# Optimization experiments

Measured on AMD Instinct MI355X. Metric: run time of the kernel, lower is better.

The kernel has to match this reference:

```python
import jax, jax.numpy as jnp
import numpy as np

D = 192   # token_dim == channel_dim == expert_dim == adapt_dim (required by source code)
S = 4096  # sequence length
NE = 8    # num_experts


def _ln(x, g, b, eps=1e-5):
    m = x.mean(-1, keepdims=True)
    v = ((x - m) ** 2).mean(-1, keepdims=True)
    return (x - m) / jnp.sqrt(v + eps) * g + b


def _adaptive(x, a, W, b, AW, Ab):
    # AdaptiveLinear with adapt_method='add': weight = W + adapt(a).view(out, in)
    dW = (AW @ a + Ab).reshape(W.shape)
    return x @ (W + dW).T + b


def setup_inputs() -> dict:
    key = jax.random.key(0)
    ks = iter(jax.random.split(key, 40))

    def n(shape, s=0.05):
        return jax.random.normal(next(ks), shape, dtype=jnp.float32) * s

    return {
        "x": n((1, S, D), 1.0),
        "W_in": n((D, D)), "b_in": n((D,)),
        "feat_W": n((D, D)), "feat_b": n((D,)),
        "feat_AW": n((D * D, D)), "feat_Ab": n((D * D,)),
        "an_g": jnp.ones((D,)), "an_b": jnp.zeros((D,)),
        "tm_W": n((D, D)), "tm_b": n((D,)),
        "tm_AW": n((D * D, D)), "tm_Ab": n((D * D,)),
        "tn_g": jnp.ones((D,)), "tn_b": jnp.zeros((D,)),
        "cm_W": n((D, D)), "cm_b": n((D,)),
        "cm_AW": n((D * D, D)), "cm_Ab": n((D * D,)),
        "cn_g": jnp.ones((D,)), "cn_b": jnp.zeros((D,)),
        "pm_W": n((D, D)), "pm_b": n((D,)),
        "gate_W": n((NE, D)), "gate_b": n((NE,)),
        "ex_W": n((NE, D, D)), "ex_b": n((NE, D)),
        "ex_AW": n((NE, D * D, D)), "ex_Ab": n((NE, D * D)),
        "mn_g": jnp.ones((D,)), "mn_b": jnp.zeros((D,)),
        "out_W": n((D, D)), "out_b": n((D,)),
    }


def reference(x, W_in, b_in, feat_W, feat_b, feat_AW, feat_Ab, an_g, an_b,
              tm_W, tm_b, tm_AW, tm_Ab, tn_g, tn_b,
              cm_W, cm_b, cm_AW, cm_Ab, cn_g, cn_b,
              pm_W, pm_b, gate_W, gate_b, ex_W, ex_b, ex_AW, ex_Ab,
              mn_g, mn_b, out_W, out_b):
    h = x @ W_in.T + b_in                                        # [1,S,D]
    xm = h.mean(axis=1)                                          # [1,D]
    a = _adaptive(xm, xm[0], feat_W, feat_b, feat_AW, feat_Ab)   # [1,D]
    a = _ln(a, an_g, an_b)
    a0 = a[0]                                                    # [D]
    t = _adaptive(h, a0, tm_W, tm_b, tm_AW, tm_Ab)               # token mixing
    t = _ln(t, tn_g, tn_b)
    c = _adaptive(t, a0, cm_W, cm_b, cm_AW, cm_Ab)               # channel mixing
    c = _ln(c, cn_g, cn_b)
    m = c @ pm_W.T + pm_b                                        # pre-MoE [1,S,D]
    gate = jax.nn.softmax(a @ gate_W.T + gate_b, axis=-1)[0]     # [NE]
    # batched hypernet weight generation for all experts at once
    dW = (jnp.einsum('eka,a->ek', ex_AW, a0) + ex_Ab).reshape(NE, D, D)
    We = ex_W + dW                                               # [NE,D,D]
    ye = jnp.einsum('bsd,ned->nbse', m, We) + ex_b[:, None, None, :]
    eo = jnp.einsum('n,nbse->bse', gate, ye)                     # soft-MoE sum
    eo = _ln(eo, mn_g, mn_b)
    eo = jax.nn.relu(eo)
    return eo @ out_W.T + out_b
```

## Files before the change

### kernel.cpp

```cpp
#include <hip/hip_runtime.h>

#define DD 192

template <int EMIT, int LNL>
__global__ __launch_bounds__(256) void stage2_k(
    const float* __restrict__ A, const float* __restrict__ W,
    const float* __restrict__ bias,
    const float* __restrict__ stats_in, const float* __restrict__ lng,
    const float* __restrict__ lnb,
    float* __restrict__ out, float* __restrict__ emit_buf) {
    __shared__ float WT[DD * 64];
    __shared__ float At[DD * 18];
    __shared__ float ms[16], rs[16];
    __shared__ float csum[4 * 64];

    const int t = threadIdx.x;
    const int tr = t >> 5, tc = t & 31;
    const int b = blockIdx.x;
    const int c0 = (b % 3) * 64;
    const int r0 = (b / 3) * 16;

    if (LNL > 0) {
        if (t < 16) {
            float s = stats_in[2 * (r0 + t)];
            float q = stats_in[2 * (r0 + t) + 1];
            float mean = s * (1.f / 192.f);
            float var = q * (1.f / 192.f) - mean * mean;
            ms[t] = mean;
            rs[t] = rsqrtf(var + 1e-5f);
        }
        __syncthreads();
    }

    {
        const float4* A4 = (const float4*)(A + (size_t)r0 * DD);
#pragma unroll
        for (int q = 0; q < 3; q++) {
            int fidx = t + 256 * q;
            int r = fidx / 48, jj = fidx - r * 48;
            float4 v = A4[fidx];
            if (LNL > 0) {
                float mean = ms[r], rstd = rs[r];
                float4 g4 = ((const float4*)lng)[jj];
                float4 b4 = ((const float4*)lnb)[jj];
                v.x = (v.x - mean) * rstd * g4.x + b4.x;
                v.y = (v.y - mean) * rstd * g4.y + b4.y;
                v.z = (v.z - mean) * rstd * g4.z + b4.z;
                v.w = (v.w - mean) * rstd * g4.w + b4.w;
                if (LNL == 2) {
                    v.x = fmaxf(v.x, 0.f); v.y = fmaxf(v.y, 0.f);
                    v.z = fmaxf(v.z, 0.f); v.w = fmaxf(v.w, 0.f);
                }
            }
            int j0 = 4 * jj;
            At[(j0 + 0) * 18 + r] = v.x;
            At[(j0 + 1) * 18 + r] = v.y;
            At[(j0 + 2) * 18 + r] = v.z;
            At[(j0 + 3) * 18 + r] = v.w;
        }
    }
    {
        const float4* W4 = (const float4*)(W + (size_t)c0 * DD);
#pragma unroll
        for (int q = 0; q < 12; q++) {
            int fidx = t + 256 * q;
            int ip = fidx / 48, jj = fidx - ip * 48;
            float4 v = W4[fidx];
            int j0 = 4 * jj;
            WT[(j0 + 0) * 64 + ((ip + 2 * ((j0 + 0) & 31)) & 63)] = v.x;
            WT[(j0 + 1) * 64 + ((ip + 2 * ((j0 + 1) & 31)) & 63)] = v.y;
            WT[(j0 + 2) * 64 + ((ip + 2 * ((j0 + 2) & 31)) & 63)] = v.z;
            WT[(j0 + 3) * 64 + ((ip + 2 * ((j0 + 3) & 31)) & 63)] = v.w;
        }
    }

    const int i0 = c0 + 2 * tc;
    float b0v = bias[i0], b1v = bias[i0 + 1];
    float acc00 = b0v, acc01 = b1v, acc10 = b0v, acc11 = b1v;
    __syncthreads();

#pragma unroll 4
    for (int j = 0; j < DD; j++) {
        float2 a2 = *(const float2*)&At[j * 18 + 2 * tr];
        int cs = (2 * tc + 2 * (j & 31)) & 63;
        float2 w2 = *(const float2*)&WT[j * 64 + cs];
        acc00 = fmaf(a2.x, w2.x, acc00);
        acc01 = fmaf(a2.x, w2.y, acc01);
        acc10 = fmaf(a2.y, w2.x, acc10);
        acc11 = fmaf(a2.y, w2.y, acc11);
    }

    const int ra = r0 + 2 * tr, rb = ra + 1;
    *(float2*)&out[(size_t)ra * DD + i0] = make_float2(acc00, acc01);
    *(float2*)&out[(size_t)rb * DD + i0] = make_float2(acc10, acc11);

    if (EMIT == 2) {
        float s0 = acc00 + acc01, q0 = acc00 * acc00 + acc01 * acc01;
        float s1 = acc10 + acc11, q1 = acc10 * acc10 + acc11 * acc11;
#pragma unroll
        for (int m = 16; m >= 1; m >>= 1) {
            s0 += __shfl_xor(s0, m); q0 += __shfl_xor(q0, m);
            s1 += __shfl_xor(s1, m); q1 += __shfl_xor(q1, m);
        }
        if (tc == 0) {
            atomicAdd(&emit_buf[2 * ra], s0);
            atomicAdd(&emit_buf[2 * ra + 1], q0);
            atomicAdd(&emit_buf[2 * rb], s1);
            atomicAdd(&emit_buf[2 * rb + 1], q1);
        }
    } else if (EMIT == 1) {
        float cs0 = acc00 + acc10;
        float cs1 = acc01 + acc11;
        cs0 += __shfl_xor(cs0, 32);
        cs1 += __shfl_xor(cs1, 32);
        int w = t >> 6;
        if ((t & 63) < 32) {
            csum[w * 64 + 2 * tc] = cs0;
            csum[w * 64 + 2 * tc + 1] = cs1;
        }
        __syncthreads();
        if (t < 64) {
            float s = csum[t] + csum[64 + t] + csum[128 + t] + csum[192 + t];
            atomicAdd(&emit_buf[c0 + t], s);
        }
    }
}

__global__ __launch_bounds__(256) void hyper_k(
    const float* __restrict__ tm_W, const float* __restrict__ tm_AW,
    const float* __restrict__ tm_Ab, const float* __restrict__ cm_W,
    const float* __restrict__ cm_AW, const float* __restrict__ cm_Ab,
    const float* __restrict__ ex_W, const float* __restrict__ ex_AW,
    const float* __restrict__ ex_Ab, const float* __restrict__ a0g,
    const float* __restrict__ gateg, float* __restrict__ Wt,
    float* __restrict__ Wc, float* __restrict__ Wmoe) {
    __shared__ float a0s[DD];
    __shared__ float rows[32 * 204];
    __shared__ float wb[32], ab[32], vals[32];
    const int t = threadIdx.x;
    const int b = blockIdx.x;
    const float* AW; const float* WB; const float* AB;
    int k0, mode, e = 0;
    if (b < 1152)      { mode = 0; AW = tm_AW; WB = tm_W; AB = tm_Ab; k0 = b * 32; }
    else if (b < 2304) { mode = 1; AW = cm_AW; WB = cm_W; AB = cm_Ab; k0 = (b - 1152) * 32; }
    else {
        mode = 2; int bb = b - 2304; e = bb / 1152; k0 = (bb - e * 1152) * 32;
        AW = ex_AW + (size_t)e * 36864 * DD;
        WB = ex_W + (size_t)e * 36864;
        AB = ex_Ab + (size_t)e * 36864;
    }
    if (t < DD) a0s[t] = a0g[t];
    if (t < 32) { wb[t] = WB[k0 + t]; ab[t] = AB[k0 + t]; }
    const float4* src4 = (const float4*)(AW + (size_t)k0 * DD);
#pragma unroll
    for (int q = 0; q < 6; q++) {
        int fidx = t + 256 * q;
        int r = fidx / 48, jj = fidx - r * 48;
        float4 v = src4[fidx];
        *(float4*)&rows[r * 204 + 4 * jj] = v;
    }
    __syncthreads();
    const int r = t >> 3, p = t & 7;
    float acc = 0.f;
#pragma unroll
    for (int q = 0; q < 6; q++) {
        int jo = p * 24 + 4 * q;
        float4 w = *(const float4*)&rows[r * 204 + jo];
        float4 aa = *(const float4*)&a0s[jo];
        acc = fmaf(w.x, aa.x, acc); acc = fmaf(w.y, aa.y, acc);
        acc = fmaf(w.z, aa.z, acc); acc = fmaf(w.w, aa.w, acc);
    }
    acc += __shfl_xor(acc, 1);
    acc += __shfl_xor(acc, 2);
    acc += __shfl_xor(acc, 4);
    if (p == 0) vals[r] = acc + wb[r] + ab[r];
    __syncthreads();
    if (t < 32) {
        if (mode == 0) Wt[k0 + t] = vals[t];
        else if (mode == 1) Wc[k0 + t] = vals[t];
        else atomicAdd(&Wmoe[k0 + t], gateg[e] * vals[t]);
    }
}

__global__ __launch_bounds__(256) void feat2_k(
    const float* __restrict__ feat_W, const float* __restrict__ feat_AW,
    const float* __restrict__ feat_Ab, const float* __restrict__ xm_sum,
    float* __restrict__ a_pre) {
    __shared__ float xms[DD];
    __shared__ float rows[32 * 204];
    __shared__ float wb[32], ab[32], vals[32];
    const int t = threadIdx.x;
    const int k0 = blockIdx.x * 32;
    if (t < DD) xms[t] = xm_sum[t] * (1.f / 4096.f);
    if (t < 32) { wb[t] = feat_W[k0 + t]; ab[t] = feat_Ab[k0 + t]; }
    const float4* src4 = (const float4*)(feat_AW + (size_t)k0 * DD);
#pragma unroll
    for (int q = 0; q < 6; q++) {
        int fidx = t + 256 * q;
        int r = fidx / 48, jj = fidx - r * 48;
        float4 v = src4[fidx];
        *(float4*)&rows[r * 204 + 4 * jj] = v;
    }
    __syncthreads();
    const int r = t >> 3, p = t & 7;
    float acc = 0.f;
#pragma unroll
    for (int q = 0; q < 6; q++) {
        int jo = p * 24 + 4 * q;
        float4 w = *(const float4*)&rows[r * 204 + jo];
        float4 aa = *(const float4*)&xms[jo];
        acc = fmaf(w.x, aa.x, acc); acc = fmaf(w.y, aa.y, acc);
        acc = fmaf(w.z, aa.z, acc); acc = fmaf(w.w, aa.w, acc);
    }
    acc += __shfl_xor(acc, 1);
    acc += __shfl_xor(acc, 2);
    acc += __shfl_xor(acc, 4);
    if (p == 0) vals[r] = acc + wb[r] + ab[r];
    __syncthreads();
    const int j0 = k0 % DD;
    if (t < 32) {
        float c = vals[t] * xms[j0 + t];
#pragma unroll
        for (int m = 16; m >= 1; m >>= 1) c += __shfl_xor(c, m);
        if (t == 0) atomicAdd(&a_pre[k0 / DD], c);
    }
}

__global__ __launch_bounds__(192) void vec_k(
    const float* __restrict__ a_pre, const float* __restrict__ feat_b,
    const float* __restrict__ an_g, const float* __restrict__ an_b,
    const float* __restrict__ gate_W, const float* __restrict__ gate_b,
    const float* __restrict__ ex_b, float* __restrict__ a0g,
    float* __restrict__ gateg, float* __restrict__ b_moe) {
    __shared__ float lgs[8];
    __shared__ float red[6];
    const int t = threadIdx.x;
    float v = a_pre[t] + feat_b[t];
    float s = v, q = v * v;
#pragma unroll
    for (int m = 32; m >= 1; m >>= 1) {
        s += __shfl_xor(s, m);
        q += __shfl_xor(q, m);
    }
    if ((t & 63) == 0) { red[t >> 6] = s; red[3 + (t >> 6)] = q; }
    if (t < 8) lgs[t] = gate_b[t];
    __syncthreads();
    float S = red[0] + red[1] + red[2];
    float Q = red[3] + red[4] + red[5];
    float mean = S * (1.f / 192.f);
    float var = Q * (1.f / 192.f) - mean * mean;
    float rstd = rsqrtf(var + 1e-5f);
    float a0v = (v - mean) * rstd * an_g[t] + an_b[t];
    a0g[t] = a0v;
#pragma unroll
    for (int e = 0; e < 8; e++) atomicAdd(&lgs[e], a0v * gate_W[e * DD + t]);
    __syncthreads();
    if (t == 0) {
        float mx = lgs[0];
        for (int e = 1; e < 8; e++) mx = fmaxf(mx, lgs[e]);
        float sum = 0.f, ex[8];
        for (int e = 0; e < 8; e++) { ex[e] = expf(lgs[e] - mx); sum += ex[e]; }
        for (int e = 0; e < 8; e++) lgs[e] = ex[e] / sum;
    }
    __syncthreads();
    if (t < 8) gateg[t] = lgs[t];
    float bm = 0.f;
#pragma unroll
    for (int e = 0; e < 8; e++) bm = fmaf(lgs[e], ex_b[e * DD + t], bm);
    b_moe[t] = bm;
}

extern "C" void kernel_launch(void* const* d_in, const int* in_sizes, int n_in,
                              void* d_out, int out_size, void* d_ws, size_t ws_size,
                              hipStream_t stream) {
    (void)in_sizes; (void)n_in; (void)out_size; (void)ws_size;
    const float* x       = (const float*)d_in[0];
    const float* W_in    = (const float*)d_in[1];
    const float* b_in    = (const float*)d_in[2];
    const float* feat_W  = (const float*)d_in[3];
    const float* feat_b  = (const float*)d_in[4];
    const float* feat_AW = (const float*)d_in[5];
    const float* feat_Ab = (const float*)d_in[6];
    const float* an_g    = (const float*)d_in[7];
    const float* an_b    = (const float*)d_in[8];
    const float* tm_W    = (const float*)d_in[9];
    const float* tm_b    = (const float*)d_in[10];
    const float* tm_AW   = (const float*)d_in[11];
    const float* tm_Ab   = (const float*)d_in[12];
    const float* tn_g    = (const float*)d_in[13];
    const float* tn_b    = (const float*)d_in[14];
    const float* cm_W    = (const float*)d_in[15];
    const float* cm_b    = (const float*)d_in[16];
    const float* cm_AW   = (const float*)d_in[17];
    const float* cm_Ab   = (const float*)d_in[18];
    const float* cn_g    = (const float*)d_in[19];
    const float* cn_b    = (const float*)d_in[20];
    const float* pm_W    = (const float*)d_in[21];
    const float* pm_b    = (const float*)d_in[22];
    const float* gate_W  = (const float*)d_in[23];
    const float* gate_b  = (const float*)d_in[24];
    const float* ex_W    = (const float*)d_in[25];
    const float* ex_b    = (const float*)d_in[26];
    const float* ex_AW   = (const float*)d_in[27];
    const float* ex_Ab   = (const float*)d_in[28];
    const float* mn_g    = (const float*)d_in[29];
    const float* mn_b    = (const float*)d_in[30];
    const float* out_W   = (const float*)d_in[31];
    const float* out_b   = (const float*)d_in[32];

    float* ws = (float*)d_ws;
    float* B0     = ws;
    float* B1     = ws + 786432;
    float* xm_sum = ws + 1572864;
    float* a_pre  = ws + 1573056;
    float* st1    = ws + 1573248;
    float* st2    = ws + 1581440;
    float* st3    = ws + 1589632;
    float* Wmoe   = ws + 1597824;
    float* Wt     = ws + 1634688;
    float* Wc     = ws + 1671552;
    float* a0     = ws + 1708416;
    float* gate   = ws + 1708608;
    float* b_moe  = ws + 1708616;

    hipMemsetAsync(xm_sum, 0, (size_t)61824 * sizeof(float), stream);

    stage2_k<1, 0><<<768, 256, 0, stream>>>(x, W_in, b_in, nullptr, nullptr, nullptr,
                                            B0, xm_sum);
    feat2_k<<<1152, 256, 0, stream>>>(feat_W, feat_AW, feat_Ab, xm_sum, a_pre);
    vec_k<<<1, 192, 0, stream>>>(a_pre, feat_b, an_g, an_b, gate_W, gate_b, ex_b,
                                 a0, gate, b_moe);
    hyper_k<<<11520, 256, 0, stream>>>(tm_W, tm_AW, tm_Ab, cm_W, cm_AW, cm_Ab,
                                       ex_W, ex_AW, ex_Ab, a0, gate, Wt, Wc, Wmoe);
    stage2_k<2, 0><<<768, 256, 0, stream>>>(B0, Wt, tm_b, nullptr, nullptr, nullptr,
                                            B1, st1);
    stage2_k<2, 1><<<768, 256, 0, stream>>>(B1, Wc, cm_b, st1, tn_g, tn_b, B0, st2);
    stage2_k<0, 1><<<768, 256, 0, stream>>>(B0, pm_W, pm_b, st2, cn_g, cn_b, B1, nullptr);
    stage2_k<2, 0><<<768, 256, 0, stream>>>(B1, Wmoe, b_moe, nullptr, nullptr, nullptr,
                                            B0, st3);
    stage2_k<0, 2><<<768, 256, 0, stream>>>(B0, out_W, out_b, st3, mn_g, mn_b,
                                            (float*)d_out, nullptr);
}
```

Measured before the change: 566.9 us.

## Double row tile to 32 and replace LN-stat atomics with per-column-group partials

The GEMM kernel now processes 32 rows per block, with each thread computing a 4x2 output tile, so each weight load from shared memory is reused across four rows and the grid halves to 384 blocks. The A tile is stored row-major with padding instead of transposed. Row sum and sum-of-squares statistics are written as three per-column-group partials and summed by the consumer, replacing the atomic adds. The memset shrinks accordingly. Costs are more shared memory per block, more registers, and fewer blocks, which lowers parallelism across the GPU's CUs.

```diff
diff --git a/kernel.cpp b/kernel.cpp
--- a/kernel.cpp
+++ b/kernel.cpp
@@ -3,27 +3,30 @@
 #define DD 192
 
 template <int EMIT, int LNL>
-__global__ __launch_bounds__(256) void stage2_k(
+__global__ __launch_bounds__(256) void stage3_k(
     const float* __restrict__ A, const float* __restrict__ W,
     const float* __restrict__ bias,
     const float* __restrict__ stats_in, const float* __restrict__ lng,
     const float* __restrict__ lnb,
     float* __restrict__ out, float* __restrict__ emit_buf) {
+    __shared__ float At[32 * 200];
     __shared__ float WT[DD * 64];
-    __shared__ float At[DD * 18];
-    __shared__ float ms[16], rs[16];
+    __shared__ float ms[32], rs[32];
     __shared__ float csum[4 * 64];
 
     const int t = threadIdx.x;
     const int tr = t >> 5, tc = t & 31;
     const int b = blockIdx.x;
-    const int c0 = (b % 3) * 64;
-    const int r0 = (b / 3) * 16;
+    const int cg = b % 3;
+    const int c0 = cg * 64;
+    const int r0 = (b / 3) * 32;
 
     if (LNL > 0) {
-        if (t < 16) {
-            float s = stats_in[2 * (r0 + t)];
-            float q = stats_in[2 * (r0 + t) + 1];
+        if (t < 32) {
+            int r = r0 + t;
+            float s = stats_in[2 * r] + stats_in[8192 + 2 * r] + stats_in[16384 + 2 * r];
+            float q = stats_in[2 * r + 1] + stats_in[8192 + 2 * r + 1]
+                    + stats_in[16384 + 2 * r + 1];
             float mean = s * (1.f / 192.f);
             float var = q * (1.f / 192.f) - mean * mean;
             ms[t] = mean;
@@ -35,10 +38,10 @@
     {
         const float4* A4 = (const float4*)(A + (size_t)r0 * DD);
 #pragma unroll
-        for (int q = 0; q < 3; q++) {
-            int fidx = t + 256 * q;
-            int r = fidx / 48, jj = fidx - r * 48;
-            float4 v = A4[fidx];
+        for (int q = 0; q < 6; q++) {
+            int f = t + 256 * q;
+            int r = f / 48, jj = f - r * 48;
+            float4 v = A4[f];
             if (LNL > 0) {
                 float mean = ms[r], rstd = rs[r];
                 float4 g4 = ((const float4*)lng)[jj];
@@ -52,20 +55,16 @@
                     v.z = fmaxf(v.z, 0.f); v.w = fmaxf(v.w, 0.f);
                 }
             }
-            int j0 = 4 * jj;
-            At[(j0 + 0) * 18 + r] = v.x;
-            At[(j0 + 1) * 18 + r] = v.y;
-            At[(j0 + 2) * 18 + r] = v.z;
-            At[(j0 + 3) * 18 + r] = v.w;
+            *(float4*)&At[r * 200 + 4 * jj] = v;
         }
     }
     {
         const float4* W4 = (const float4*)(W + (size_t)c0 * DD);
 #pragma unroll
         for (int q = 0; q < 12; q++) {
-            int fidx = t + 256 * q;
-            int ip = fidx / 48, jj = fidx - ip * 48;
-            float4 v = W4[fidx];
+            int f = t + 256 * q;
+            int ip = f / 48, jj = f - ip * 48;
+            float4 v = W4[f];
             int j0 = 4 * jj;
             WT[(j0 + 0) * 64 + ((ip + 2 * ((j0 + 0) & 31)) & 63)] = v.x;
             WT[(j0 + 1) * 64 + ((ip + 2 * ((j0 + 1) & 31)) & 63)] = v.y;
@@ -75,42 +74,52 @@
     }
 
     const int i0 = c0 + 2 * tc;
-    float b0v = bias[i0], b1v = bias[i0 + 1];
-    float acc00 = b0v, acc01 = b1v, acc10 = b0v, acc11 = b1v;
-    __syncthreads();
-
+    float bv0 = bias[i0], bv1 = bias[i0 + 1];
+    float acc[4][2];
+#pragma unroll
+    for (int i = 0; i < 4; i++) { acc[i][0] = bv0; acc[i][1] = bv1; }
+    __syncthreads();
+
+    const int rbase = 4 * tr;
 #pragma unroll 4
     for (int j = 0; j < DD; j++) {
-        float2 a2 = *(const float2*)&At[j * 18 + 2 * tr];
         int cs = (2 * tc + 2 * (j & 31)) & 63;
         float2 w2 = *(const float2*)&WT[j * 64 + cs];
-        acc00 = fmaf(a2.x, w2.x, acc00);
-        acc01 = fmaf(a2.x, w2.y, acc01);
-        acc10 = fmaf(a2.y, w2.x, acc10);
-        acc11 = fmaf(a2.y, w2.y, acc11);
-    }
-
-    const int ra = r0 + 2 * tr, rb = ra + 1;
-    *(float2*)&out[(size_t)ra * DD + i0] = make_float2(acc00, acc01);
-    *(float2*)&out[(size_t)rb * DD + i0] = make_float2(acc10, acc11);
+        float a0 = At[(rbase + 0) * 200 + j];
+        float a1 = At[(rbase + 1) * 200 + j];
+        float a2 = At[(rbase + 2) * 200 + j];
+        float a3 = At[(rbase + 3) * 200 + j];
+        acc[0][0] = fmaf(a0, w2.x, acc[0][0]); acc[0][1] = fmaf(a0, w2.y, acc[0][1]);
+        acc[1][0] = fmaf(a1, w2.x, acc[1][0]); acc[1][1] = fmaf(a1, w2.y, acc[1][1]);
+        acc[2][0] = fmaf(a2, w2.x, acc[2][0]); acc[2][1] = fmaf(a2, w2.y, acc[2][1]);
+        acc[3][0] = fmaf(a3, w2.x, acc[3][0]); acc[3][1] = fmaf(a3, w2.y, acc[3][1]);
+    }
+
+#pragma unroll
+    for (int i = 0; i < 4; i++) {
+        int row = r0 + rbase + i;
+        *(float2*)&out[(size_t)row * DD + i0] = make_float2(acc[i][0], acc[i][1]);
+    }
 
     if (EMIT == 2) {
-        float s0 = acc00 + acc01, q0 = acc00 * acc00 + acc01 * acc01;
-        float s1 = acc10 + acc11, q1 = acc10 * acc10 + acc11 * acc11;
-#pragma unroll
-        for (int m = 16; m >= 1; m >>= 1) {
-            s0 += __shfl_xor(s0, m); q0 += __shfl_xor(q0, m);
-            s1 += __shfl_xor(s1, m); q1 += __shfl_xor(q1, m);
-        }
-        if (tc == 0) {
-            atomicAdd(&emit_buf[2 * ra], s0);
-            atomicAdd(&emit_buf[2 * ra + 1], q0);
-            atomicAdd(&emit_buf[2 * rb], s1);
-            atomicAdd(&emit_buf[2 * rb + 1], q1);
+#pragma unroll
+        for (int i = 0; i < 4; i++) {
+            float s = acc[i][0] + acc[i][1];
+            float q = acc[i][0] * acc[i][0] + acc[i][1] * acc[i][1];
+#pragma unroll
+            for (int m = 16; m >= 1; m >>= 1) {
+                s += __shfl_xor(s, m);
+                q += __shfl_xor(q, m);
+            }
+            if (tc == 0) {
+                int r = r0 + rbase + i;
+                emit_buf[cg * 8192 + 2 * r] = s;
+                emit_buf[cg * 8192 + 2 * r + 1] = q;
+            }
         }
     } else if (EMIT == 1) {
-        float cs0 = acc00 + acc10;
-        float cs1 = acc01 + acc11;
+        float cs0 = acc[0][0] + acc[1][0] + acc[2][0] + acc[3][0];
+        float cs1 = acc[0][1] + acc[1][1] + acc[2][1] + acc[3][1];
         cs0 += __shfl_xor(cs0, 32);
         cs1 += __shfl_xor(cs1, 32);
         int w = t >> 6;
@@ -313,31 +322,31 @@
     float* B1     = ws + 786432;
     float* xm_sum = ws + 1572864;
     float* a_pre  = ws + 1573056;
-    float* st1    = ws + 1573248;
-    float* st2    = ws + 1581440;
-    float* st3    = ws + 1589632;
-    float* Wmoe   = ws + 1597824;
-    float* Wt     = ws + 1634688;
-    float* Wc     = ws + 1671552;
-    float* a0     = ws + 1708416;
-    float* gate   = ws + 1708608;
-    float* b_moe  = ws + 1708616;
-
-    hipMemsetAsync(xm_sum, 0, (size_t)61824 * sizeof(float), stream);
-
-    stage2_k<1, 0><<<768, 256, 0, stream>>>(x, W_in, b_in, nullptr, nullptr, nullptr,
+    float* Wmoe   = ws + 1573248;
+    float* Wt     = ws + 1610112;
+    float* Wc     = ws + 1646976;
+    float* st1    = ws + 1683840;
+    float* st2    = ws + 1708416;
+    float* st3    = ws + 1732992;
+    float* a0     = ws + 1757568;
+    float* gate   = ws + 1757760;
+    float* b_moe  = ws + 1757768;
+
+    hipMemsetAsync(xm_sum, 0, (size_t)37248 * sizeof(float), stream);
+
+    stage3_k<1, 0><<<384, 256, 0, stream>>>(x, W_in, b_in, nullptr, nullptr, nullptr,
                                             B0, xm_sum);
     feat2_k<<<1152, 256, 0, stream>>>(feat_W, feat_AW, feat_Ab, xm_sum, a_pre);
     vec_k<<<1, 192, 0, stream>>>(a_pre, feat_b, an_g, an_b, gate_W, gate_b, ex_b,
                                  a0, gate, b_moe);
     hyper_k<<<11520, 256, 0, stream>>>(tm_W, tm_AW, tm_Ab, cm_W, cm_AW, cm_Ab,
                                        ex_W, ex_AW, ex_Ab, a0, gate, Wt, Wc, Wmoe);
-    stage2_k<2, 0><<<768, 256, 0, stream>>>(B0, Wt, tm_b, nullptr, nullptr, nullptr,
+    stage3_k<2, 0><<<384, 256, 0, stream>>>(B0, Wt, tm_b, nullptr, nullptr, nullptr,
                                             B1, st1);
-    stage2_k<2, 1><<<768, 256, 0, stream>>>(B1, Wc, cm_b, st1, tn_g, tn_b, B0, st2);
-    stage2_k<0, 1><<<768, 256, 0, stream>>>(B0, pm_W, pm_b, st2, cn_g, cn_b, B1, nullptr);
-    stage2_k<2, 0><<<768, 256, 0, stream>>>(B1, Wmoe, b_moe, nullptr, nullptr, nullptr,
+    stage3_k<2, 1><<<384, 256, 0, stream>>>(B1, Wc, cm_b, st1, tn_g, tn_b, B0, st2);
+    stage3_k<0, 1><<<384, 256, 0, stream>>>(B0, pm_W, pm_b, st2, cn_g, cn_b, B1, nullptr);
+    stage3_k<2, 0><<<384, 256, 0, stream>>>(B1, Wmoe, b_moe, nullptr, nullptr, nullptr,
                                             B0, st3);
-    stage2_k<0, 2><<<768, 256, 0, stream>>>(B0, out_W, out_b, st3, mn_g, mn_b,
+    stage3_k<0, 2><<<384, 256, 0, stream>>>(B0, out_W, out_b, st3, mn_g, mn_b,
                                             (float*)d_out, nullptr);
 }
```

Measured after the change: 537.1 us. 1.06x faster.
